# Kernel optimization log

Measured on AMD Instinct MI355X. Metric: run time of the kernel, lower is better.

## Reference

```python
import jax, jax.numpy as jnp
import numpy as np
import math

H = 16          # num_heads
EPS = 1e-5      # LayerNorm eps (torch default)


def setup_inputs() -> dict:
    key = jax.random.key(0)
    ks = jax.random.split(key, 4)
    B, T, D = 2, 2048, 1024
    s = 1.0 / math.sqrt(D)
    return {
        "x": jax.random.normal(ks[0], (B, T, D), dtype=jnp.float32),
        "ln_g": jnp.ones((D,), jnp.float32),
        "ln_b": jnp.zeros((D,), jnp.float32),
        "Wq": jax.random.normal(ks[1], (D, D), jnp.float32) * s,
        "bq": jnp.zeros((D,), jnp.float32),
        "Wk": jax.random.normal(ks[2], (D, D), jnp.float32) * s,
        "bk": jnp.zeros((D,), jnp.float32),
        "Wv": jax.random.normal(ks[3], (D, D), jnp.float32) * s,
        "bv": jnp.zeros((D,), jnp.float32),
    }


def reference(x, ln_g, ln_b, Wq, bq, Wk, bk, Wv, bv):
    B, T, D = x.shape
    # LayerNorm (shared across the three projections, computed once)
    mu = jnp.mean(x, axis=-1, keepdims=True)
    var = jnp.mean(jnp.square(x - mu), axis=-1, keepdims=True)
    xn = (x - mu) * jax.lax.rsqrt(var + EPS) * ln_g + ln_b
    # Q/K/V projections -> [B, T, H, Dh]
    q = (xn @ Wq + bq).reshape(B, T, H, D // H)
    k = (xn @ Wk + bk).reshape(B, T, H, D // H)
    v = (xn @ Wv + bv).reshape(B, T, H, D // H)
    # QK^T scores [B, n, m, h], scaled by sqrt(head_dim)
    scale = 1.0 / math.sqrt(D // H)
    attn = jnp.einsum('bnhd,bmhd->bnmh', q, k) * scale
    # softmax over key axis (dim=2), dropout p=0 is identity
    w = jax.nn.softmax(attn, axis=2)
    # weighted sum of values, merge heads
    y = jnp.einsum('bnmh,bmhd->bnhd', w, v).reshape(B, T, D)
    return y
```

## Files before the change

kernel.cpp:

```cpp
#include <hip/hip_runtime.h>
#include <hip/hip_bf16.h>


typedef __attribute__((ext_vector_type(8)))  short short8;
typedef __attribute__((ext_vector_type(4)))  float f32x4;
typedef __attribute__((ext_vector_type(2)))  float f32x2;
typedef __attribute__((ext_vector_type(16))) float f32x16;
typedef __attribute__((ext_vector_type(2)))  unsigned int uint2v;

#define D_MODEL 1024
#define T_SEQ   2048
#define NHEAD   16
#define HDIM    64

#define LOG2E 1.4426950408889634f

__device__ __forceinline__ unsigned short f2bf(float x) {
    unsigned int u = __float_as_uint(x);
    u = (u + 0x7fffu + ((u >> 16) & 1u)) >> 16;
    return (unsigned short)u;
}

#if defined(__has_builtin)
#if __has_builtin(__builtin_amdgcn_permlane32_swap)
#define HAVE_PERMSWAP 1
#endif
#endif

__device__ __forceinline__ uint2v permswap(unsigned a, unsigned b) {
#ifdef HAVE_PERMSWAP
    return __builtin_amdgcn_permlane32_swap(a, b, false, false);
#else
    uint2v r;
    const unsigned as = (unsigned)__shfl_xor((int)a, 32, 64);
    const unsigned bs = (unsigned)__shfl_xor((int)b, 32, 64);
    const bool hi = (threadIdx.x & 32) != 0;
    r[0] = hi ? bs : a;
    r[1] = hi ? b  : as;
    return r;
#endif
}

__device__ __forceinline__ void group_barrier() {
    asm volatile("s_waitcnt lgkmcnt(0)" ::: "memory");
    __builtin_amdgcn_s_barrier();
    asm volatile("" ::: "memory");
}

__device__ __forceinline__ void w8(unsigned short* p, const uint4 v) {
    uint2 a; a.x = v.x; a.y = v.y;
    uint2 b; b.x = v.z; b.y = v.w;
    *(uint2*)p = a;
    *(uint2*)(p + 4) = b;
}

__device__ __forceinline__ short8 read8(const unsigned short* p) {
    union { unsigned u[4]; short8 s; } r;
    const uint2 a = *(const uint2*)p;
    const uint2 b = *(const uint2*)(p + 4);
    r.u[0] = a.x; r.u[1] = a.y; r.u[2] = b.x; r.u[3] = b.y;
    return r.s;
}

__global__ __launch_bounds__(256) void ln_wcast_kernel(
    const float* __restrict__ x, const float* __restrict__ gam,
    const float* __restrict__ bet, unsigned short* __restrict__ xn,
    const float* __restrict__ Wq, const float* __restrict__ Wk,
    const float* __restrict__ Wv, unsigned short* __restrict__ Wt)
{
    __shared__ float red[8];
    __shared__ float tile[32][33];
    const int bid = blockIdx.x;
    if (bid < 4096) {
        const int row = bid;
        const int t = threadIdx.x;
        const float4 v = ((const float4*)(x + (size_t)row * D_MODEL))[t];
        float s  = v.x + v.y + v.z + v.w;
        float s2 = v.x * v.x + v.y * v.y + v.z * v.z + v.w * v.w;
#pragma unroll
        for (int off = 32; off; off >>= 1) {
            s  += __shfl_down(s,  off, 64);
            s2 += __shfl_down(s2, off, 64);
        }
        const int lane = t & 63, wave = t >> 6;
        if (lane == 0) { red[wave] = s; red[4 + wave] = s2; }
        __syncthreads();
        s  = red[0] + red[1] + red[2] + red[3];
        s2 = red[4] + red[5] + red[6] + red[7];
        const float mu   = s * (1.f / D_MODEL);
        const float var  = s2 * (1.f / D_MODEL) - mu * mu;
        const float rstd = rsqrtf(var + 1e-5f);
        const float4 gv = ((const float4*)gam)[t];
        const float4 bv = ((const float4*)bet)[t];
        ushort4 o;
        o.x = f2bf((v.x - mu) * rstd * gv.x + bv.x);
        o.y = f2bf((v.y - mu) * rstd * gv.y + bv.y);
        o.z = f2bf((v.z - mu) * rstd * gv.z + bv.z);
        o.w = f2bf((v.w - mu) * rstd * gv.w + bv.w);
        ((ushort4*)(xn + (size_t)row * D_MODEL))[t] = o;
    } else {
        const int id = bid - 4096;
        const int z  = id >> 10;
        const int t2 = id & 1023;
        const int n0 = (t2 & 31) * 32, k0 = (t2 >> 5) * 32;
        const float* W = (z == 0) ? Wq : (z == 1) ? Wk : Wv;
        unsigned short* outw = Wt + (size_t)z * D_MODEL * D_MODEL;
        const int tx = threadIdx.x & 31, ty = threadIdx.x >> 5;
#pragma unroll
        for (int i = ty; i < 32; i += 8)
            tile[i][tx] = W[(size_t)(k0 + i) * D_MODEL + n0 + tx];
        __syncthreads();
#pragma unroll
        for (int i = ty; i < 32; i += 8)
            outw[(size_t)(n0 + i) * D_MODEL + k0 + tx] = f2bf(tile[tx][i]);
    }
}

__global__ __launch_bounds__(256) void qkv_gemm_kernel(
    const unsigned short* __restrict__ xn, const unsigned short* __restrict__ Wt,
    const float* __restrict__ bq, const float* __restrict__ bk, const float* __restrict__ bv,
    unsigned short* __restrict__ qo, unsigned short* __restrict__ ko, unsigned short* __restrict__ vt)
{
    const int which = blockIdx.x >> 3;
    const int xt = blockIdx.x & 7, yt = blockIdx.y;
    const bool vmode = (which == 2);
    const unsigned short* Aptr = vmode ? (Wt + (size_t)2 * D_MODEL * D_MODEL) : xn;
    const unsigned short* Bptr = vmode ? xn : (Wt + (size_t)which * D_MODEL * D_MODEL);
    const float* bias   = (which == 0) ? bq : (which == 1) ? bk : bv;
    const float scale   = (which == 0) ? (0.125f * LOG2E) : 1.0f;
    const int m0 = vmode ? xt * 128 : yt * 128;
    const int n0 = vmode ? yt * 128 : xt * 128;

    __shared__ unsigned short As[128][32];
    __shared__ unsigned short Bs[128][32];

    const int tid = threadIdx.x;
    const int lane = tid & 63, wave = tid >> 6;
    const int wr = wave >> 1, wc = wave & 1;
    const int g = lane >> 4, c = lane & 15;

    const int srow = (lane >> 2);
    const int scol = (lane & 3) * 8;

    f32x4 acc[4][4] = {};

    for (int kt = 0; kt < D_MODEL; kt += 32) {
        __syncthreads();
#pragma unroll
        for (int i = 0; i < 2; ++i) {
            const int r = wave * 32 + i * 16;
            const unsigned short* ga = Aptr + (size_t)(m0 + r + srow) * D_MODEL + kt + scol;
            __builtin_amdgcn_global_load_lds(
                (const __attribute__((address_space(1))) unsigned int*)ga,
                (__attribute__((address_space(3))) unsigned int*)(&As[r][0]), 16, 0, 0);
            const unsigned short* gb = Bptr + (size_t)(n0 + r + srow) * D_MODEL + kt + scol;
            __builtin_amdgcn_global_load_lds(
                (const __attribute__((address_space(1))) unsigned int*)gb,
                (__attribute__((address_space(3))) unsigned int*)(&Bs[r][0]), 16, 0, 0);
        }
        __syncthreads();

        short8 af[4], bf[4];
#pragma unroll
        for (int i = 0; i < 4; ++i) {
            af[i] = *(const short8*)(&As[wr * 64 + i * 16 + c][g * 8]);
            bf[i] = *(const short8*)(&Bs[wc * 64 + i * 16 + c][g * 8]);
        }
#pragma unroll
        for (int i = 0; i < 4; ++i)
#pragma unroll
            for (int j = 0; j < 4; ++j)
                acc[i][j] = __builtin_amdgcn_mfma_f32_16x16x32_bf16(af[i], bf[j], acc[i][j], 0, 0, 0);
    }

    if (!vmode) {
        unsigned short* out = (which == 0) ? qo : ko;
#pragma unroll
        for (int j = 0; j < 4; ++j) {
            const int n = n0 + wc * 64 + j * 16 + c;
            const float bn = bias[n];
            const int h = n >> 6, dh = n & 63;
#pragma unroll
            for (int i = 0; i < 4; ++i) {
#pragma unroll
                for (int r = 0; r < 4; ++r) {
                    const int m = m0 + wr * 64 + i * 16 + g * 4 + r;
                    const int bb = m >> 11, t = m & 2047;
                    out[((size_t)(bb * NHEAD + h) * T_SEQ + t) * HDIM + dh] =
                        f2bf((acc[i][j][r] + bn) * scale);
                }
            }
        }
    } else {
#pragma unroll
        for (int i = 0; i < 4; ++i) {
#pragma unroll
            for (int r = 0; r < 4; ++r) {
                const int m = m0 + wr * 64 + i * 16 + g * 4 + r;
                const float bn = bias[m];
#pragma unroll
                for (int j = 0; j < 4; ++j) {
                    const int n = n0 + wc * 64 + j * 16 + c;
                    const int bb = n >> 11, t = n & 2047;
                    vt[(size_t)bb * (D_MODEL * T_SEQ) + (size_t)m * T_SEQ + t] =
                        f2bf(acc[i][j][r] + bn);
                }
            }
        }
    }
}

__global__ __launch_bounds__(512, 4) void attn_kernel(
    const unsigned short* __restrict__ qb, const unsigned short* __restrict__ kb,
    const unsigned short* __restrict__ vtb, float* __restrict__ out)
{
    const int id  = blockIdx.x;
    const int swz = (id & 7) * 64 + (id >> 3);
    const int qt  = swz & 15;
    const int bh  = swz >> 4;
    const int b = bh >> 4, head = bh & 15;
    const unsigned short* Q  = qb  + (size_t)bh * T_SEQ * HDIM;
    const unsigned short* Kp = kb  + (size_t)bh * T_SEQ * HDIM;
    const unsigned short* Vt = vtb + (size_t)b * (D_MODEL * T_SEQ)
                                   + (size_t)head * (HDIM * T_SEQ);

    __shared__ __align__(16) unsigned short smem[34816];

    const int tid = threadIdx.x, lane = tid & 63, wave = tid >> 6;
    const int grp = wave >> 2, w4 = wave & 3;
    const int q = lane & 31, h = lane >> 5;
    const int kvbase = grp * (T_SEQ / 2);

    const int gtid = tid & 255;
    const int sr = gtid >> 3;
    const int sc = (gtid & 7) * 8;

    unsigned short* gbase = &smem[grp * 17408];

    short8 qf[4];
    {
        const unsigned short* qp = Q + (size_t)(qt * 128 + w4 * 32 + q) * HDIM;
#pragma unroll
        for (int c = 0; c < 4; ++c)
            qf[c] = *(const short8*)(qp + c * 16 + h * 8);
    }

    float l_r = 0.f;
    f32x16 o[2] = {};

    const unsigned short* kp0 = Kp + (size_t)(kvbase + sr) * HDIM + sc;
    const unsigned short* vp0 = Vt + (size_t)sr * T_SEQ + kvbase + sc;
    uint4 kr0 = *(const uint4*)(kp0);
    uint4 kr1 = *(const uint4*)(kp0 + 32 * HDIM);
    uint4 vr0 = *(const uint4*)(vp0);
    uint4 vr1 = *(const uint4*)(vp0 + 32 * T_SEQ);
    w8(gbase + sr * 68 + sc, kr0);
    w8(gbase + (sr + 32) * 68 + sc, kr1);
    w8(gbase + 8704 + sr * 68 + sc, vr0);
    w8(gbase + 8704 + (sr + 32) * 68 + sc, vr1);
    kp0 += 64 * HDIM;
    vp0 += 64;

    int cur = 0;
#pragma unroll 1
    for (int t = 0; t < 16; ++t) {
        const bool more = (t + 1 < 16);
        if (more) {
            kr0 = *(const uint4*)(kp0);
            kr1 = *(const uint4*)(kp0 + 32 * HDIM);
            vr0 = *(const uint4*)(vp0);
            vr1 = *(const uint4*)(vp0 + 32 * T_SEQ);
            kp0 += 64 * HDIM;
            vp0 += 64;
        }
        group_barrier();
        const unsigned short* kbuf = gbase + cur * 4352;
        const unsigned short* vbuf = gbase + 8704 + cur * 4352;

        f32x16 s0 = {}, s1 = {};
        __builtin_amdgcn_s_setprio(1);
#pragma unroll
        for (int c = 0; c < 4; ++c) {
            const short8 kf0 = read8(kbuf + (size_t)q * 68 + c * 16 + h * 8);
            const short8 kf1 = read8(kbuf + (size_t)(32 + q) * 68 + c * 16 + h * 8);
            s0 = __builtin_amdgcn_mfma_f32_32x32x16_bf16(kf0, qf[c], s0, 0, 0, 0);
            s1 = __builtin_amdgcn_mfma_f32_32x32x16_bf16(kf1, qf[c], s1, 0, 0, 0);
        }
        __builtin_amdgcn_s_setprio(0);

#pragma unroll
        for (int r = 0; r < 16; ++r) { s0[r] = exp2f(s0[r]); }
#pragma unroll
        for (int r = 0; r < 16; ++r) { s1[r] = exp2f(s1[r]); }

        {
            f32x2 u[8];
#pragma unroll
            for (int r = 0; r < 8; ++r) {
                f32x2 a; a[0] = s0[2*r]; a[1] = s0[2*r+1];
                f32x2 bb; bb[0] = s1[2*r]; bb[1] = s1[2*r+1];
                u[r] = a + bb;
            }
            u[0] += u[1]; u[2] += u[3]; u[4] += u[5]; u[6] += u[7];
            u[0] += u[2]; u[4] += u[6];
            u[0] += u[4];
            float rs = u[0][0] + u[0][1];
            rs += __shfl_xor(rs, 32, 64);
            l_r += rs;
        }

        unsigned Wb0[8], Wb1[8];
#pragma unroll
        for (int u = 0; u < 4; ++u) {
            asm("v_cvt_pk_bf16_f32 %0, %1, %2" : "=v"(Wb0[u*2])   : "v"(s0[4*u]),   "v"(s0[4*u+1]));
            asm("v_cvt_pk_bf16_f32 %0, %1, %2" : "=v"(Wb0[u*2+1]) : "v"(s0[4*u+2]), "v"(s0[4*u+3]));
            asm("v_cvt_pk_bf16_f32 %0, %1, %2" : "=v"(Wb1[u*2])   : "v"(s1[4*u]),   "v"(s1[4*u+1]));
            asm("v_cvt_pk_bf16_f32 %0, %1, %2" : "=v"(Wb1[u*2+1]) : "v"(s1[4*u+2]), "v"(s1[4*u+3]));
        }

        short8 pf[4];
#pragma unroll
        for (int m = 0; m < 2; ++m) {
            {
                const uint2v r0 = permswap(Wb0[4*m],     Wb0[4*m + 2]);
                const uint2v r1 = permswap(Wb0[4*m + 1], Wb0[4*m + 3]);
                union { unsigned u[4]; short8 s; } pw;
                pw.u[0] = r0[0]; pw.u[1] = r1[0]; pw.u[2] = r0[1]; pw.u[3] = r1[1];
                pf[m] = pw.s;
            }
            {
                const uint2v r0 = permswap(Wb1[4*m],     Wb1[4*m + 2]);
                const uint2v r1 = permswap(Wb1[4*m + 1], Wb1[4*m + 3]);
                union { unsigned u[4]; short8 s; } pw;
                pw.u[0] = r0[0]; pw.u[1] = r1[0]; pw.u[2] = r0[1]; pw.u[3] = r1[1];
                pf[2 + m] = pw.s;
            }
        }

        __builtin_amdgcn_s_setprio(1);
#pragma unroll
        for (int dt = 0; dt < 2; ++dt) {
#pragma unroll
            for (int cp = 0; cp < 4; ++cp) {
                const short8 vf = read8(vbuf + (size_t)(dt * 32 + q) * 68 + cp * 16 + h * 8);
                o[dt] = __builtin_amdgcn_mfma_f32_32x32x16_bf16(vf, pf[cp], o[dt], 0, 0, 0);
            }
        }
        __builtin_amdgcn_s_setprio(0);

        if (more) {
            unsigned short* kd = gbase + (cur ^ 1) * 4352;
            unsigned short* vd = gbase + 8704 + (cur ^ 1) * 4352;
            w8(kd + sr * 68 + sc, kr0);
            w8(kd + (sr + 32) * 68 + sc, kr1);
            w8(vd + sr * 68 + sc, vr0);
            w8(vd + (sr + 32) * 68 + sc, vr1);
        }
        cur ^= 1;
    }

    __syncthreads();
    float* obuf  = (float*)(void*)smem;
    float* l_lds = ((float*)(void*)smem) + 128 * 68;

    const int qrl = w4 * 32 + q;
    if (grp == 0) {
#pragma unroll
        for (int dt = 0; dt < 2; ++dt)
#pragma unroll
            for (int u = 0; u < 4; ++u) {
                float* dst = obuf + (size_t)qrl * 68 + dt * 32 + 8 * u + 4 * h;
                float2 lo; lo.x = o[dt][4*u];     lo.y = o[dt][4*u + 1];
                float2 hi; hi.x = o[dt][4*u + 2]; hi.y = o[dt][4*u + 3];
                *(float2*)dst = lo;
                *(float2*)(dst + 2) = hi;
            }
        if (h == 0) l_lds[qrl] = l_r;
    }
    __syncthreads();
    if (grp == 1) {
        const float invl = 1.0f / (l_lds[qrl] + l_r);
#pragma unroll
        for (int dt = 0; dt < 2; ++dt)
#pragma unroll
            for (int u = 0; u < 4; ++u) {
                float* dst = obuf + (size_t)qrl * 68 + dt * 32 + 8 * u + 4 * h;
                float2 lo = *(const float2*)dst;
                float2 hi = *(const float2*)(dst + 2);
                lo.x = (lo.x + o[dt][4*u])     * invl;
                lo.y = (lo.y + o[dt][4*u + 1]) * invl;
                hi.x = (hi.x + o[dt][4*u + 2]) * invl;
                hi.y = (hi.y + o[dt][4*u + 3]) * invl;
                *(float2*)dst = lo;
                *(float2*)(dst + 2) = hi;
            }
    }
    __syncthreads();
#pragma unroll
    for (int it = 0; it < 4; ++it) {
        const int row = it * 32 + (tid >> 4);
        const int col = (tid & 15) * 4;
        const float4 v = *(const float4*)(&obuf[(size_t)row * 68 + col]);
        *(float4*)(&out[(size_t)(b * T_SEQ + qt * 128 + row) * D_MODEL + head * HDIM + col]) = v;
    }
}

extern "C" void kernel_launch(void* const* d_in, const int* in_sizes, int n_in,
                              void* d_out, int out_size, void* d_ws, size_t ws_size,
                              hipStream_t stream)
{
    const float* x   = (const float*)d_in[0];
    const float* lng = (const float*)d_in[1];
    const float* lnb = (const float*)d_in[2];
    const float* Wq  = (const float*)d_in[3];
    const float* bq  = (const float*)d_in[4];
    const float* Wk  = (const float*)d_in[5];
    const float* bk  = (const float*)d_in[6];
    const float* Wv  = (const float*)d_in[7];
    const float* bv  = (const float*)d_in[8];
    float* out = (float*)d_out;

    unsigned short* xn = (unsigned short*)d_ws;
    unsigned short* Wt = xn + (size_t)4096 * 1024;
    unsigned short* qh = Wt + (size_t)3 * 1024 * 1024;
    unsigned short* kh = qh + (size_t)4096 * 1024;
    unsigned short* vt = kh + (size_t)4096 * 1024;

    ln_wcast_kernel<<<7168, 256, 0, stream>>>(x, lng, lnb, xn, Wq, Wk, Wv, Wt);
    qkv_gemm_kernel<<<dim3(24, 32), 256, 0, stream>>>(xn, Wt, bq, bk, bv, qh, kh, vt);
    attn_kernel<<<512, 512, 0, stream>>>(qh, kh, vt, out);
}
```

Measured before the change: 112.0 us.

## Restructure attention to per-wave KV split with direct global fragment loads

Attention blocks now cover 32 query rows with 4 waves, and each wave handles a quarter of the KV sequence. K and V fragments are loaded straight from global memory into registers, which drops the LDS double-buffered staging and the per-iteration barriers. Partial outputs and row sums from the four waves are combined through shared memory at the end. The intent is to remove LDS traffic and sync overhead and to raise block count. In exchange, each K/V tile is read from global or L2 by four times as many blocks, and the loads are not overlapped with compute.

```diff
diff --git a/kernel.cpp b/kernel.cpp
--- a/kernel.cpp
+++ b/kernel.cpp
@@ -39,27 +39,6 @@
     r[1] = hi ? b  : as;
     return r;
 #endif
-}
-
-__device__ __forceinline__ void group_barrier() {
-    asm volatile("s_waitcnt lgkmcnt(0)" ::: "memory");
-    __builtin_amdgcn_s_barrier();
-    asm volatile("" ::: "memory");
-}
-
-__device__ __forceinline__ void w8(unsigned short* p, const uint4 v) {
-    uint2 a; a.x = v.x; a.y = v.y;
-    uint2 b; b.x = v.z; b.y = v.w;
-    *(uint2*)p = a;
-    *(uint2*)(p + 4) = b;
-}
-
-__device__ __forceinline__ short8 read8(const unsigned short* p) {
-    union { unsigned u[4]; short8 s; } r;
-    const uint2 a = *(const uint2*)p;
-    const uint2 b = *(const uint2*)(p + 4);
-    r.u[0] = a.x; r.u[1] = a.y; r.u[2] = b.x; r.u[3] = b.y;
-    return r.s;
 }
 
 __global__ __launch_bounds__(256) void ln_wcast_kernel(
@@ -210,36 +189,30 @@
     }
 }
 
-__global__ __launch_bounds__(512, 4) void attn_kernel(
+__global__ __launch_bounds__(256) void attn_kernel(
     const unsigned short* __restrict__ qb, const unsigned short* __restrict__ kb,
     const unsigned short* __restrict__ vtb, float* __restrict__ out)
 {
     const int id  = blockIdx.x;
-    const int swz = (id & 7) * 64 + (id >> 3);
-    const int qt  = swz & 15;
-    const int bh  = swz >> 4;
+    const int swz = (id & 7) * 256 + (id >> 3);
+    const int bh  = swz >> 6;
+    const int qt  = swz & 63;
     const int b = bh >> 4, head = bh & 15;
     const unsigned short* Q  = qb  + (size_t)bh * T_SEQ * HDIM;
     const unsigned short* Kp = kb  + (size_t)bh * T_SEQ * HDIM;
     const unsigned short* Vt = vtb + (size_t)b * (D_MODEL * T_SEQ)
                                    + (size_t)head * (HDIM * T_SEQ);
 
-    __shared__ __align__(16) unsigned short smem[34816];
+    __shared__ float obuf[4][32][68];
+    __shared__ float l_lds[4][32];
 
     const int tid = threadIdx.x, lane = tid & 63, wave = tid >> 6;
-    const int grp = wave >> 2, w4 = wave & 3;
     const int q = lane & 31, h = lane >> 5;
-    const int kvbase = grp * (T_SEQ / 2);
-
-    const int gtid = tid & 255;
-    const int sr = gtid >> 3;
-    const int sc = (gtid & 7) * 8;
-
-    unsigned short* gbase = &smem[grp * 17408];
+    const int kvbase = wave * (T_SEQ / 4);
 
     short8 qf[4];
     {
-        const unsigned short* qp = Q + (size_t)(qt * 128 + w4 * 32 + q) * HDIM;
+        const unsigned short* qp = Q + (size_t)(qt * 32 + q) * HDIM;
 #pragma unroll
         for (int c = 0; c < 4; ++c)
             qf[c] = *(const short8*)(qp + c * 16 + h * 8);
@@ -248,45 +221,30 @@
     float l_r = 0.f;
     f32x16 o[2] = {};
 
-    const unsigned short* kp0 = Kp + (size_t)(kvbase + sr) * HDIM + sc;
-    const unsigned short* vp0 = Vt + (size_t)sr * T_SEQ + kvbase + sc;
-    uint4 kr0 = *(const uint4*)(kp0);
-    uint4 kr1 = *(const uint4*)(kp0 + 32 * HDIM);
-    uint4 vr0 = *(const uint4*)(vp0);
-    uint4 vr1 = *(const uint4*)(vp0 + 32 * T_SEQ);
-    w8(gbase + sr * 68 + sc, kr0);
-    w8(gbase + (sr + 32) * 68 + sc, kr1);
-    w8(gbase + 8704 + sr * 68 + sc, vr0);
-    w8(gbase + 8704 + (sr + 32) * 68 + sc, vr1);
-    kp0 += 64 * HDIM;
-    vp0 += 64;
-
-    int cur = 0;
-#pragma unroll 1
-    for (int t = 0; t < 16; ++t) {
-        const bool more = (t + 1 < 16);
-        if (more) {
-            kr0 = *(const uint4*)(kp0);
-            kr1 = *(const uint4*)(kp0 + 32 * HDIM);
-            vr0 = *(const uint4*)(vp0);
-            vr1 = *(const uint4*)(vp0 + 32 * T_SEQ);
-            kp0 += 64 * HDIM;
-            vp0 += 64;
-        }
-        group_barrier();
-        const unsigned short* kbuf = gbase + cur * 4352;
-        const unsigned short* vbuf = gbase + 8704 + cur * 4352;
+    const unsigned short* kp = Kp + (size_t)(kvbase + q) * HDIM + h * 8;
+    const unsigned short* vp = Vt + (size_t)q * T_SEQ + kvbase + h * 8;
+
+#pragma unroll 2
+    for (int t = 0; t < 8; ++t) {
+        const int kv0 = t * 64;
+        short8 kf0[4], kf1[4], vf0[4], vf1[4];
+#pragma unroll
+        for (int c = 0; c < 4; ++c) {
+            kf0[c] = *(const short8*)(kp + (size_t)(kv0 + 0)  * HDIM + c * 16);
+            kf1[c] = *(const short8*)(kp + (size_t)(kv0 + 32) * HDIM + c * 16);
+        }
+#pragma unroll
+        for (int cp = 0; cp < 4; ++cp) {
+            vf0[cp] = *(const short8*)(vp + kv0 + cp * 16);
+            vf1[cp] = *(const short8*)(vp + (size_t)32 * T_SEQ + kv0 + cp * 16);
+        }
 
         f32x16 s0 = {}, s1 = {};
-        __builtin_amdgcn_s_setprio(1);
 #pragma unroll
         for (int c = 0; c < 4; ++c) {
-            const short8 kf0 = read8(kbuf + (size_t)q * 68 + c * 16 + h * 8);
-            const short8 kf1 = read8(kbuf + (size_t)(32 + q) * 68 + c * 16 + h * 8);
-            s0 = __builtin_amdgcn_mfma_f32_32x32x16_bf16(kf0, qf[c], s0, 0, 0, 0);
-            s1 = __builtin_amdgcn_mfma_f32_32x32x16_bf16(kf1, qf[c], s1, 0, 0, 0);
-        }
-        __builtin_amdgcn_s_setprio(0);
+            s0 = __builtin_amdgcn_mfma_f32_32x32x16_bf16(kf0[c], qf[c], s0, 0, 0, 0);
+            s1 = __builtin_amdgcn_mfma_f32_32x32x16_bf16(kf1[c], qf[c], s1, 0, 0, 0);
+        }
 
 #pragma unroll
         for (int r = 0; r < 16; ++r) { s0[r] = exp2f(s0[r]); }
@@ -337,71 +295,47 @@
             }
         }
 
-        __builtin_amdgcn_s_setprio(1);
-#pragma unroll
-        for (int dt = 0; dt < 2; ++dt) {
-#pragma unroll
-            for (int cp = 0; cp < 4; ++cp) {
-                const short8 vf = read8(vbuf + (size_t)(dt * 32 + q) * 68 + cp * 16 + h * 8);
-                o[dt] = __builtin_amdgcn_mfma_f32_32x32x16_bf16(vf, pf[cp], o[dt], 0, 0, 0);
-            }
-        }
-        __builtin_amdgcn_s_setprio(0);
-
-        if (more) {
-            unsigned short* kd = gbase + (cur ^ 1) * 4352;
-            unsigned short* vd = gbase + 8704 + (cur ^ 1) * 4352;
-            w8(kd + sr * 68 + sc, kr0);
-            w8(kd + (sr + 32) * 68 + sc, kr1);
-            w8(vd + sr * 68 + sc, vr0);
-            w8(vd + (sr + 32) * 68 + sc, vr1);
-        }
-        cur ^= 1;
-    }
-
+#pragma unroll
+        for (int cp = 0; cp < 4; ++cp) {
+            o[0] = __builtin_amdgcn_mfma_f32_32x32x16_bf16(vf0[cp], pf[cp], o[0], 0, 0, 0);
+            o[1] = __builtin_amdgcn_mfma_f32_32x32x16_bf16(vf1[cp], pf[cp], o[1], 0, 0, 0);
+        }
+    }
+
+#pragma unroll
+    for (int dt = 0; dt < 2; ++dt)
+#pragma unroll
+        for (int u = 0; u < 4; ++u) {
+            float* dst = &obuf[wave][q][dt * 32 + 8 * u + 4 * h];
+            float2 lo; lo.x = o[dt][4*u];     lo.y = o[dt][4*u + 1];
+            float2 hi; hi.x = o[dt][4*u + 2]; hi.y = o[dt][4*u + 3];
+            *(float2*)dst = lo;
+            *(float2*)(dst + 2) = hi;
+        }
+    if (h == 0) l_lds[wave][q] = l_r;
     __syncthreads();
-    float* obuf  = (float*)(void*)smem;
-    float* l_lds = ((float*)(void*)smem) + 128 * 68;
-
-    const int qrl = w4 * 32 + q;
-    if (grp == 0) {
-#pragma unroll
-        for (int dt = 0; dt < 2; ++dt)
-#pragma unroll
-            for (int u = 0; u < 4; ++u) {
-                float* dst = obuf + (size_t)qrl * 68 + dt * 32 + 8 * u + 4 * h;
-                float2 lo; lo.x = o[dt][4*u];     lo.y = o[dt][4*u + 1];
-                float2 hi; hi.x = o[dt][4*u + 2]; hi.y = o[dt][4*u + 3];
-                *(float2*)dst = lo;
-                *(float2*)(dst + 2) = hi;
-            }
-        if (h == 0) l_lds[qrl] = l_r;
-    }
-    __syncthreads();
-    if (grp == 1) {
-        const float invl = 1.0f / (l_lds[qrl] + l_r);
-#pragma unroll
-        for (int dt = 0; dt < 2; ++dt)
-#pragma unroll
-            for (int u = 0; u < 4; ++u) {
-                float* dst = obuf + (size_t)qrl * 68 + dt * 32 + 8 * u + 4 * h;
-                float2 lo = *(const float2*)dst;
-                float2 hi = *(const float2*)(dst + 2);
-                lo.x = (lo.x + o[dt][4*u])     * invl;
-                lo.y = (lo.y + o[dt][4*u + 1]) * invl;
-                hi.x = (hi.x + o[dt][4*u + 2]) * invl;
-                hi.y = (hi.y + o[dt][4*u + 3]) * invl;
-                *(float2*)dst = lo;
-                *(float2*)(dst + 2) = hi;
-            }
-    }
-    __syncthreads();
-#pragma unroll
-    for (int it = 0; it < 4; ++it) {
-        const int row = it * 32 + (tid >> 4);
-        const int col = (tid & 15) * 4;
-        const float4 v = *(const float4*)(&obuf[(size_t)row * 68 + col]);
-        *(float4*)(&out[(size_t)(b * T_SEQ + qt * 128 + row) * D_MODEL + head * HDIM + col]) = v;
+
+    {
+        const int row = tid >> 3;
+        const int col = (tid & 7) * 8;
+        const float invl = 1.0f / (l_lds[0][row] + l_lds[1][row] +
+                                   l_lds[2][row] + l_lds[3][row]);
+        float acc[8];
+#pragma unroll
+        for (int e = 0; e < 8; ++e) acc[e] = 0.f;
+#pragma unroll
+        for (int w = 0; w < 4; ++w) {
+            const float4 a = *(const float4*)(&obuf[w][row][col]);
+            const float4 bq4 = *(const float4*)(&obuf[w][row][col + 4]);
+            acc[0] += a.x; acc[1] += a.y; acc[2] += a.z; acc[3] += a.w;
+            acc[4] += bq4.x; acc[5] += bq4.y; acc[6] += bq4.z; acc[7] += bq4.w;
+        }
+        float4 r0, r1;
+        r0.x = acc[0] * invl; r0.y = acc[1] * invl; r0.z = acc[2] * invl; r0.w = acc[3] * invl;
+        r1.x = acc[4] * invl; r1.y = acc[5] * invl; r1.z = acc[6] * invl; r1.w = acc[7] * invl;
+        float* op = &out[(size_t)(b * T_SEQ + qt * 32 + row) * D_MODEL + head * HDIM + col];
+        *(float4*)op = r0;
+        *(float4*)(op + 4) = r1;
     }
 }
 
@@ -428,5 +362,5 @@
 
     ln_wcast_kernel<<<7168, 256, 0, stream>>>(x, lng, lnb, xn, Wq, Wk, Wv, Wt);
     qkv_gemm_kernel<<<dim3(24, 32), 256, 0, stream>>>(xn, Wt, bq, bk, bv, qh, kh, vt);
-    attn_kernel<<<512, 512, 0, stream>>>(qh, kh, vt, out);
-}
+    attn_kernel<<<2048, 256, 0, stream>>>(qh, kh, vt, out);
+}
```

New measurement: 179.0 us. 59.8% more time.
